# Kernel tuning notes

Hardware: AMD Instinct MI355X
Metric: run time of the kernel (lower is better)

## Reference

```python
import jax, jax.numpy as jnp
import numpy as np

N = 50000
E = 300000
F_IN, H, OUT = 100, 256, 512
L = 3


def _lin(key, fan_in, fan_out):
    k1, k2 = jax.random.split(key)
    lim = 1.0 / np.sqrt(fan_in)
    W = jax.random.uniform(k1, (fan_in, fan_out), minval=-lim, maxval=lim, dtype=jnp.float32)
    b = jax.random.uniform(k2, (fan_out,), minval=-lim, maxval=lim, dtype=jnp.float32)
    return W, b


def setup_inputs() -> dict:
    key = jax.random.key(0)
    ks = jax.random.split(key, 12)
    x = jax.random.normal(ks[0], (N, F_IN), dtype=jnp.float32)
    edge_index = jax.random.randint(ks[1], (2, E), 0, N, dtype=jnp.int64)
    edge_attr = jax.random.uniform(ks[2], (E,), dtype=jnp.float32)
    Wi, bi = _lin(ks[3], F_IN, H)
    gW, gb = [], []
    for i in range(L):
        W, b = _lin(ks[4 + i], H, H)
        gW.append(W); gb.append(b)
    Wg = jnp.stack(gW)  # [L, H, H]
    bg = jnp.stack(gb)  # [L, H]
    Wo1, bo1 = _lin(ks[7], H, 2 * H)
    Wo2, bo2 = _lin(ks[8], 2 * H, OUT)
    Wh1, bh1 = _lin(ks[9], OUT, 256)
    Wh2, bh2 = _lin(ks[10], 256, 128)
    Wh3, bh3 = _lin(ks[11], 128, 5)
    return {"x": x, "edge_index": edge_index, "edge_attr": edge_attr,
            "target_species_idx": 0,
            "Wi": Wi, "bi": bi, "Wg": Wg, "bg": bg,
            "Wo1": Wo1, "bo1": bo1, "Wo2": Wo2, "bo2": bo2,
            "Wh1": Wh1, "bh1": bh1, "Wh2": Wh2, "bh2": bh2, "Wh3": Wh3, "bh3": bh3}


def _gcn_conv(x, W, b, row, col, norm):
    # PyG GCNConv: x' = D^-1/2 (A+I) D^-1/2 (x W) + b (norm precomputed)
    h = x @ W                                   # [N, H]
    msg = norm[:, None] * h[row]                # gather sources  [E+N, H]
    out = jnp.zeros_like(h).at[col].add(msg)    # scatter to targets
    return out + b


def reference(x, edge_index, edge_attr, target_species_idx,
              Wi, bi, Wg, bg, Wo1, bo1, Wo2, bo2,
              Wh1, bh1, Wh2, bh2, Wh3, bh3):
    n = x.shape[0]
    loop = jnp.arange(n, dtype=edge_index.dtype)
    row = jnp.concatenate([edge_index[0], loop])   # sources (with self-loops)
    col = jnp.concatenate([edge_index[1], loop])   # targets
    ew = jnp.concatenate([edge_attr, jnp.ones((n,), dtype=x.dtype)])
    deg = jnp.zeros((n,), dtype=x.dtype).at[col].add(ew)
    dinv = jnp.where(deg > 0, jax.lax.rsqrt(deg), 0.0)
    norm = dinv[row] * ew * dinv[col]              # [E+N]

    h = jax.nn.relu(x @ Wi + bi)
    for i in range(L):
        h = _gcn_conv(h, Wg[i], bg[i], row, col, norm)
        if i < L - 1:
            h = jax.nn.relu(h)  # dropout is identity in eval mode
    h = jax.nn.relu(h @ Wo1 + bo1) @ Wo2 + bo2     # output_proj [N, OUT]
    t = h[target_species_idx]                      # [OUT]
    t = jax.nn.relu(t @ Wh1 + bh1)
    t = jax.nn.relu(t @ Wh2 + bh2)
    return t @ Wh3 + bh3                           # [5]
```

## Files before the change

kernel.cpp:

```cpp
#include <hip/hip_runtime.h>

#define HDIM 256
#define CAPN 4096
#define MAXDEG 64
#define NT 256


__device__ __forceinline__ float4 fma4(float s, float4 w, float4 a) {
  a.x = fmaf(s, w.x, a.x); a.y = fmaf(s, w.y, a.y);
  a.z = fmaf(s, w.z, a.z); a.w = fmaf(s, w.w, a.w);
  return a;
}

__device__ __forceinline__ int detect_stride(const int* __restrict__ ei, int E,
                                             int* s_st, int tid) {
  if (tid < 64) {
    bool nz = (tid < E) && (ei[2 * tid + 1] != 0);
    unsigned long long b = __ballot(nz);
    if (tid == 0) *s_st = (b != 0ULL) ? 1 : 2;
  }
  __syncthreads();
  return *s_st;
}

__device__ __forceinline__ void load_cols4(const int* __restrict__ ei, int E, int e0,
                                           int st, int c[4]) {
  if (st == 1) {
    int4 v = *(const int4*)&ei[E + e0];
    c[0] = v.x; c[1] = v.y; c[2] = v.z; c[3] = v.w;
  } else {
    int4 v1 = *(const int4*)&ei[(size_t)(E + e0) * 2];
    int4 v2 = *(const int4*)&ei[(size_t)(E + e0) * 2 + 4];
    c[0] = v1.x; c[1] = v1.z; c[2] = v2.x; c[3] = v2.z;
  }
}

__global__ void k_init(int* __restrict__ map, float* __restrict__ deg,
                       int* __restrict__ meta, int* __restrict__ nodeof,
                       int* __restrict__ dcnt, const int* __restrict__ tgt, int N) {
  int t = tgt[0];
  int gtid = blockIdx.x * blockDim.x + threadIdx.x, gsz = gridDim.x * blockDim.x;
  int4* m4 = (int4*)map;
  float4* d4 = (float4*)deg;
  int nv = N >> 2, tv = t >> 2, tl = t & 3;
  for (int i = gtid; i < nv; i += gsz) {
    int4 z = {0, 0, 0, 0};
    if (i == tv) (&z.x)[tl] = 7;
    m4[i] = z;
    d4[i] = make_float4(0.f, 0.f, 0.f, 0.f);
  }
  for (int i = (nv << 2) + gtid; i < N; i += gsz) { map[i] = (i == t) ? 7 : 0; deg[i] = 0.f; }
  int4* c4 = (int4*)dcnt;
  for (int i = gtid; i < 3 * CAPN / 4; i += gsz) c4[i] = make_int4(0, 0, 0, 0);
  if (gtid == 0) { meta[0] = 1; meta[10] = 0; nodeof[0] = t; }
}

__device__ __forceinline__ void expand_edge(const int* __restrict__ ei, int E, int st,
                                            int e, int mv, int l, int* __restrict__ meta,
                                            int* __restrict__ map, int* __restrict__ nodeof,
                                            int* __restrict__ dcnt, int* __restrict__ dstl) {
  if (mv >= 4 && (mv & 3) >= l) {
    int sv = (mv >> 2) - 1;
    int idx = atomicAdd(&dcnt[sv], 1);
    if (idx < MAXDEG) dstl[sv * MAXDEG + idx] = e;
    else atomicOr(&meta[10], 1);
    int r = ei[(size_t)e * st];
    if (atomicCAS(&map[r], 0, 1) == 0) {
      int ns = atomicAdd(&meta[0], 1);
      if (ns < CAPN) { nodeof[ns] = r; map[r] = ((ns + 1) << 2) | (l - 1); }
    }
  }
}

#define DEGB 128
__global__ void k_deg_exp3(const int* __restrict__ ei, const float* __restrict__ ea,
                           int E, int* __restrict__ meta, int* __restrict__ map,
                           int* __restrict__ nodeof, int* __restrict__ dcnt2,
                           int* __restrict__ dstl2, float* __restrict__ deg) {
  __shared__ int s_st;
  int tid = threadIdx.x;
  int st = detect_stride(ei, E, &s_st, tid);
  if (blockIdx.x < DEGB) {
    int stride = DEGB * NT * 4;
    for (int e0 = (blockIdx.x * NT + tid) * 4; e0 < E; e0 += stride) {
      int ne = E - e0;
      if (ne >= 4) {
        int c[4]; load_cols4(ei, E, e0, st, c);
        float4 w = *(const float4*)&ea[e0];
        atomicAdd(&deg[c[0]], w.x); atomicAdd(&deg[c[1]], w.y);
        atomicAdd(&deg[c[2]], w.z); atomicAdd(&deg[c[3]], w.w);
      } else {
        for (int k = 0; k < ne; ++k)
          atomicAdd(&deg[ei[(size_t)(E + e0 + k) * st]], ea[e0 + k]);
      }
    }
  } else {
    int stride = DEGB * NT * 4;
    for (int e0 = ((blockIdx.x - DEGB) * NT + tid) * 4; e0 < E; e0 += stride) {
      int ne = E - e0;
      if (ne >= 4) {
        int c[4]; load_cols4(ei, E, e0, st, c);
        for (int k = 0; k < 4; ++k)
          expand_edge(ei, E, st, e0 + k, map[c[k]], 3, meta, map, nodeof, dcnt2, dstl2);
      } else {
        for (int k = 0; k < ne; ++k) {
          int c = ei[(size_t)(E + e0 + k) * st];
          expand_edge(ei, E, st, e0 + k, map[c], 3, meta, map, nodeof, dcnt2, dstl2);
        }
      }
    }
  }
}

__global__ void k_exp4(const int* __restrict__ ei, int E, int* __restrict__ meta,
                       int* __restrict__ map, int* __restrict__ nodeof,
                       int* __restrict__ dcnt, int* __restrict__ dstl, int l) {
  __shared__ int s_st;
  int tid = threadIdx.x;
  int st = detect_stride(ei, E, &s_st, tid);
  int e0 = (blockIdx.x * NT + tid) * 4;
  if (e0 >= E) return;
  int ne = E - e0;
  if (ne >= 4) {
    int c[4]; load_cols4(ei, E, e0, st, c);
    for (int k = 0; k < 4; ++k)
      expand_edge(ei, E, st, e0 + k, map[c[k]], l, meta, map, nodeof, dcnt, dstl);
  } else {
    for (int k = 0; k < ne; ++k) {
      int c = ei[(size_t)(E + e0 + k) * st];
      expand_edge(ei, E, st, e0 + k, map[c], l, meta, map, nodeof, dcnt, dstl);
    }
  }
}

__global__ void __launch_bounds__(NT) k_l0q(
    const int* __restrict__ meta, const int* __restrict__ nodeof,
    const float* __restrict__ x, const float* __restrict__ Wi,
    const float* __restrict__ bi, const float* __restrict__ W0,
    float* __restrict__ gout) {
  __shared__ float xs[4][112];
  __shared__ float hs[4][HDIM];
  __shared__ float4 red[4][4][64];
  const float4* Wi4 = (const float4*)Wi;
  const float4* W04 = (const float4*)W0;
  const float4* bi4 = (const float4*)bi;
  float4* g4 = (float4*)gout;
  int ntot = meta[0]; if (ntot > CAPN) ntot = CAPN;
  int tid = threadIdx.x, q = tid & 63, kg = tid >> 6;
  for (int base = blockIdx.x * 4; base < ntot; base += gridDim.x * 4) {
    int nr = ntot - base; if (nr > 4) nr = 4;
    for (int idx = tid; idx < nr * 100; idx += NT) {
      int r = idx / 100, k2 = idx - r * 100;
      xs[r][k2] = x[(size_t)nodeof[base + r] * 100 + k2];
    }
    __syncthreads();
    {
      float4 a0 = {0,0,0,0}, a1 = a0, a2 = a0, a3 = a0;
#pragma unroll 5
      for (int k2 = kg * 25; k2 < kg * 25 + 25; ++k2) {
        float4 w = Wi4[(size_t)k2 * 64 + q];
        a0 = fma4(xs[0][k2], w, a0); a1 = fma4(xs[1][k2], w, a1);
        a2 = fma4(xs[2][k2], w, a2); a3 = fma4(xs[3][k2], w, a3);
      }
      red[0][kg][q] = a0; red[1][kg][q] = a1; red[2][kg][q] = a2; red[3][kg][q] = a3;
    }
    __syncthreads();
    if (tid < 64) {
      float4 bb = bi4[tid];
      for (int r = 0; r < nr; ++r) {
        float4 s = red[r][0][tid], s1 = red[r][1][tid], s2 = red[r][2][tid], s3 = red[r][3][tid];
        s.x = fmaxf(s.x + s1.x + s2.x + s3.x + bb.x, 0.0f);
        s.y = fmaxf(s.y + s1.y + s2.y + s3.y + bb.y, 0.0f);
        s.z = fmaxf(s.z + s1.z + s2.z + s3.z + bb.z, 0.0f);
        s.w = fmaxf(s.w + s1.w + s2.w + s3.w + bb.w, 0.0f);
        *(float4*)&hs[r][tid * 4] = s;
      }
    }
    __syncthreads();
    {
      float4 a0 = {0,0,0,0}, a1 = a0, a2 = a0, a3 = a0;
#pragma unroll 4
      for (int m = kg * 64; m < kg * 64 + 64; ++m) {
        float4 w = W04[(size_t)m * 64 + q];
        a0 = fma4(hs[0][m], w, a0); a1 = fma4(hs[1][m], w, a1);
        a2 = fma4(hs[2][m], w, a2); a3 = fma4(hs[3][m], w, a3);
      }
      red[0][kg][q] = a0; red[1][kg][q] = a1; red[2][kg][q] = a2; red[3][kg][q] = a3;
    }
    __syncthreads();
    if (tid < 64) {
      for (int r = 0; r < nr; ++r) {
        float4 s = red[r][0][tid], s1 = red[r][1][tid], s2 = red[r][2][tid], s3 = red[r][3][tid];
        s.x += s1.x + s2.x + s3.x; s.y += s1.y + s2.y + s3.y;
        s.z += s1.z + s2.z + s3.z; s.w += s1.w + s2.w + s3.w;
        g4[(size_t)(base + r) * 64 + tid] = s;
      }
    }
    __syncthreads();
  }
}

__global__ void __launch_bounds__(NT) k_gv(
    const int* __restrict__ meta, int kk, const int* __restrict__ map,
    const int* __restrict__ nodeof, const int* __restrict__ ei, int E,
    const float* __restrict__ ea, const float* __restrict__ deg,
    const int* __restrict__ dcnt, const int* __restrict__ dstl,
    const float* __restrict__ gprev, const float* __restrict__ W,
    const float* __restrict__ bprev, float* __restrict__ gout) {
  __shared__ int s_st;
  __shared__ float hs[4][HDIM];
  __shared__ float4 red[4][4][64];
  __shared__ int   sul[4][MAXDEG];
  __shared__ float nrml[4][MAXDEG];
  __shared__ float dvr[4];
  __shared__ int   ml[4];
  int tid = threadIdx.x;
  int st = detect_stride(ei, E, &s_st, tid);
  const float4* W4 = (const float4*)W;
  const float4* b4 = (const float4*)bprev;
  const float4* gp4 = (const float4*)gprev;
  float4* go4 = (float4*)gout;
  int ntot = meta[0]; if (ntot > CAPN) ntot = CAPN;
  int q = tid & 63, kg = tid >> 6;
  for (int base = blockIdx.x * 4; base < ntot; base += gridDim.x * 4) {
    int nr = ntot - base; if (nr > 4) nr = 4;
    int maxb = -1;
    for (int r = 0; r < nr; ++r) maxb = max(maxb, map[nodeof[base + r]] & 3);
    if (maxb < kk) continue;
    {
      int r = tid >> 6, i = tid & 63;
      if (r < nr) {
        int s = base + r;
        int m = dcnt[s]; if (m > MAXDEG) m = MAXDEG;
        if (i == 0) { ml[r] = m; dvr[r] = 1.0f / sqrtf(deg[nodeof[s]] + 1.0f); }
        if (i < m) {
          int e = dstl[s * MAXDEG + i];
          int u = ei[(size_t)e * st];
          int mu = map[u];
          sul[r][i] = (mu >= 4) ? (mu >> 2) - 1 : 0;
          nrml[r][i] = (mu >= 4) ? (1.0f / sqrtf(deg[u] + 1.0f)) * ea[e] : 0.0f;
        }
      }
    }
    __syncthreads();
    for (int idx = tid; idx < nr * 64; idx += NT) {
      int r = idx >> 6, qq = idx & 63;
      int s = base + r;
      float dv = dvr[r], d2 = dv * dv;
      float4 gs = gp4[(size_t)s * 64 + qq];
      float4 acc = b4[qq];
      acc.x = fmaf(d2, gs.x, acc.x); acc.y = fmaf(d2, gs.y, acc.y);
      acc.z = fmaf(d2, gs.z, acc.z); acc.w = fmaf(d2, gs.w, acc.w);
      float4 ms = {0,0,0,0};
      int m = ml[r];
      for (int i = 0; i < m; ++i)
        ms = fma4(nrml[r][i], gp4[(size_t)sul[r][i] * 64 + qq], ms);
      acc.x = fmaxf(fmaf(dv, ms.x, acc.x), 0.0f);
      acc.y = fmaxf(fmaf(dv, ms.y, acc.y), 0.0f);
      acc.z = fmaxf(fmaf(dv, ms.z, acc.z), 0.0f);
      acc.w = fmaxf(fmaf(dv, ms.w, acc.w), 0.0f);
      *(float4*)&hs[r][qq * 4] = acc;
    }
    __syncthreads();
    {
      float4 a0 = {0,0,0,0}, a1 = a0, a2 = a0, a3 = a0;
#pragma unroll 4
      for (int m = kg * 64; m < kg * 64 + 64; ++m) {
        float4 w = W4[(size_t)m * 64 + q];
        a0 = fma4(hs[0][m], w, a0); a1 = fma4(hs[1][m], w, a1);
        a2 = fma4(hs[2][m], w, a2); a3 = fma4(hs[3][m], w, a3);
      }
      red[0][kg][q] = a0; red[1][kg][q] = a1; red[2][kg][q] = a2; red[3][kg][q] = a3;
    }
    __syncthreads();
    if (tid < 64) {
      for (int r = 0; r < nr; ++r) {
        float4 s = red[r][0][tid], s1 = red[r][1][tid], s2 = red[r][2][tid], s3 = red[r][3][tid];
        s.x += s1.x + s2.x + s3.x; s.y += s1.y + s2.y + s3.y;
        s.z += s1.z + s2.z + s3.z; s.w += s1.w + s2.w + s3.w;
        go4[(size_t)(base + r) * 64 + tid] = s;
      }
    }
    __syncthreads();
  }
}

__global__ void __launch_bounds__(NT) k_heads1(
    const int* __restrict__ ei, int E, const float* __restrict__ ea,
    const int* __restrict__ map, const int* __restrict__ nodeof,
    const int* __restrict__ dcnt2, const int* __restrict__ dstl2,
    const float* __restrict__ deg, const float* __restrict__ b2,
    const float* __restrict__ g2, const float* __restrict__ Wo1,
    const float* __restrict__ bo1, float* __restrict__ v1) {
  __shared__ int s_st;
  __shared__ float h3[256];
  __shared__ float4 red[256];
  __shared__ int   sul[MAXDEG];
  __shared__ float nrml[MAXDEG];
  int tid = threadIdx.x;
  int st = detect_stride(ei, E, &s_st, tid);
  int t = nodeof[0];
  float dvt = 1.0f / sqrtf(deg[t] + 1.0f);
  int m = dcnt2[0]; if (m > MAXDEG) m = MAXDEG;
  if (tid < m) {
    int e = dstl2[tid];
    int u = ei[(size_t)e * st];
    int mu = map[u];
    sul[tid] = (mu >= 4) ? (mu >> 2) - 1 : 0;
    nrml[tid] = (mu >= 4) ? (1.0f / sqrtf(deg[u] + 1.0f)) * ea[e] : 0.0f;
  }
  __syncthreads();
  {
    float acc = b2[tid] + dvt * dvt * g2[tid];
    float ms = 0.0f;
    for (int i = 0; i < m; ++i)
      ms = fmaf(nrml[i], g2[(size_t)sul[i] * HDIM + tid], ms);
    h3[tid] = fmaf(dvt, ms, acc);
  }
  __syncthreads();
  int q = tid & 15, kg = tid >> 4;
  const float4* W4 = (const float4*)Wo1;
  int quad = blockIdx.x * 16 + q;
  float4 a = {0,0,0,0};
#pragma unroll
  for (int k = kg * 16; k < kg * 16 + 16; ++k)
    a = fma4(h3[k], W4[(size_t)k * 128 + quad], a);
  red[kg * 16 + q] = a;
  __syncthreads();
  if (tid < 16) {
    float4 s = red[tid];
    for (int g = 1; g < 16; ++g) {
      float4 r = red[g * 16 + tid];
      s.x += r.x; s.y += r.y; s.z += r.z; s.w += r.w;
    }
    float4 bb = ((const float4*)bo1)[blockIdx.x * 16 + tid];
    s.x = fmaxf(s.x + bb.x, 0.f); s.y = fmaxf(s.y + bb.y, 0.f);
    s.z = fmaxf(s.z + bb.z, 0.f); s.w = fmaxf(s.w + bb.w, 0.f);
    ((float4*)v1)[blockIdx.x * 16 + tid] = s;
  }
}

template <int KIN, int KOUT, int BLOCKS, bool RELU>
__global__ void __launch_bounds__(NT) k_headv(const float* __restrict__ vin,
                                              const float* __restrict__ W,
                                              const float* __restrict__ b,
                                              float* __restrict__ vout) {
  constexpr int QPB = KOUT / (4 * BLOCKS);
  constexpr int KG = 256 / QPB;
  constexpr int KQ = KIN / KG;
  __shared__ float vs[KIN];
  __shared__ float4 red[256];
  int tid = threadIdx.x;
  for (int k = tid; k < KIN; k += NT) vs[k] = vin[k];
  __syncthreads();
  int q = tid % QPB, kg = tid / QPB;
  const float4* W4 = (const float4*)W;
  int quad = blockIdx.x * QPB + q;
  float4 a = {0,0,0,0};
#pragma unroll 8
  for (int k = kg * KQ; k < kg * KQ + KQ; ++k)
    a = fma4(vs[k], W4[(size_t)k * (KOUT / 4) + quad], a);
  red[kg * QPB + q] = a;
  __syncthreads();
  if (tid < QPB) {
    float4 s = red[tid];
    for (int g = 1; g < KG; ++g) {
      float4 r = red[g * QPB + tid];
      s.x += r.x; s.y += r.y; s.z += r.z; s.w += r.w;
    }
    float4 bb = ((const float4*)b)[blockIdx.x * QPB + tid];
    s.x += bb.x; s.y += bb.y; s.z += bb.z; s.w += bb.w;
    if (RELU) {
      s.x = fmaxf(s.x, 0.f); s.y = fmaxf(s.y, 0.f);
      s.z = fmaxf(s.z, 0.f); s.w = fmaxf(s.w, 0.f);
    }
    ((float4*)vout)[blockIdx.x * QPB + tid] = s;
  }
}

__global__ void __launch_bounds__(NT) k_tailq(
    const float* __restrict__ vin, const float* __restrict__ Wh2,
    const float* __restrict__ bh2, const float* __restrict__ Wh3,
    const float* __restrict__ bh3, const int* __restrict__ meta,
    float* __restrict__ out) {
  __shared__ float vs[256];
  __shared__ float4 red[256];
  __shared__ float v4s[128];
  int tid = threadIdx.x;
  vs[tid] = vin[tid];
  __syncthreads();
  int q = tid & 31, kg = tid >> 5;
  const float4* W4 = (const float4*)Wh2;
  float4 a = {0,0,0,0};
#pragma unroll 8
  for (int k = kg * 32; k < kg * 32 + 32; ++k)
    a = fma4(vs[k], W4[(size_t)k * 32 + q], a);
  red[kg * 32 + q] = a;
  __syncthreads();
  if (tid < 32) {
    float4 s = red[tid];
    for (int g = 1; g < 8; ++g) {
      float4 r = red[g * 32 + tid];
      s.x += r.x; s.y += r.y; s.z += r.z; s.w += r.w;
    }
    float4 bb = ((const float4*)bh2)[tid];
    *(float4*)&v4s[tid * 4] = make_float4(fmaxf(s.x + bb.x, 0.f), fmaxf(s.y + bb.y, 0.f),
                                          fmaxf(s.z + bb.z, 0.f), fmaxf(s.w + bb.w, 0.f));
  }
  __syncthreads();
  if (tid < 5) {
    float a2 = bh3[tid];
#pragma unroll 4
    for (int k = 0; k < 128; ++k) a2 = fmaf(v4s[k], Wh3[k * 5 + tid], a2);
    if (tid == 4) {
      int B = 0;
      if (meta[0] > CAPN) B |= 1;
      if (meta[10] != 0) B |= 2;
      if (B) a2 = 1.0e6f * (float)B;
    }
    out[tid] = a2;
  }
}

__global__ void k_diag(float* __restrict__ out, float D) {
  int tid = threadIdx.x;
  if (tid < 4) out[tid] = 0.0f;
  if (tid == 4) out[tid] = D;
}

extern "C" void kernel_launch(void* const* d_in, const int* in_sizes, int n_in,
                              void* d_out, int out_size, void* d_ws, size_t ws_size,
                              hipStream_t stream) {
  float* out = (float*)d_out;

  static const long long EXP[18] = {5000000, 600000, 300000, 1, 25600, 256, 196608, 768,
                                    131072, 512, 262144, 512, 131072, 256, 32768, 128, 640, 5};
  if (n_in != 18) {
    k_diag<<<1, 64, 0, stream>>>(out, 3.0e6f + 1000.0f * (float)n_in);
    return;
  }
  for (int i = 0; i < 18; ++i) {
    long long s = in_sizes[i];
    bool ok = (s == EXP[i]) || (i == 1 && s == 2 * EXP[1]);
    if (!ok) {
      k_diag<<<1, 64, 0, stream>>>(out, (float)(i + 1) * 1.0e5f);
      return;
    }
  }

  const float* x   = (const float*)d_in[0];
  const int*   ei  = (const int*)d_in[1];
  const float* ea  = (const float*)d_in[2];
  const int*   tgt = (const int*)d_in[3];
  const float* Wi  = (const float*)d_in[4];
  const float* bi  = (const float*)d_in[5];
  const float* Wg  = (const float*)d_in[6];
  const float* bg  = (const float*)d_in[7];
  const float* Wo1 = (const float*)d_in[8];
  const float* bo1 = (const float*)d_in[9];
  const float* Wo2 = (const float*)d_in[10];
  const float* bo2 = (const float*)d_in[11];
  const float* Wh1 = (const float*)d_in[12];
  const float* bh1 = (const float*)d_in[13];
  const float* Wh2 = (const float*)d_in[14];
  const float* bh2 = (const float*)d_in[15];
  const float* Wh3 = (const float*)d_in[16];
  const float* bh3 = (const float*)d_in[17];

  const int N = 50000, E = 300000;

  auto al = [](size_t b) { return (b + 255) & ~(size_t)255; };
  char* ws = (char*)d_ws;
  size_t off = 0;
  auto alloc = [&](size_t bytes) { char* p = ws + off; off += al(bytes); return p; };

  int*   map    = (int*)alloc((size_t)N * 4);
  int*   meta   = (int*)alloc(256);
  float* deg    = (float*)alloc((size_t)N * 4);
  int*   nodeof = (int*)alloc((size_t)CAPN * 4);
  int*   dcnt   = (int*)alloc((size_t)3 * CAPN * 4);
  int*   dstl   = (int*)alloc((size_t)3 * CAPN * MAXDEG * 4);
  float* gA     = (float*)alloc((size_t)CAPN * HDIM * 4);
  float* gB     = (float*)alloc((size_t)CAPN * HDIM * 4);
  float* headv  = (float*)alloc(8192);
  float* v1 = headv;
  float* v2 = headv + 512;
  float* v3 = headv + 1024;

  if (off > ws_size) {
    k_diag<<<1, 64, 0, stream>>>(out, 9.0e6f + (float)(ws_size >> 20));
    return;
  }

  int* dcnt0 = dcnt;               int* dstl0 = dstl;
  int* dcnt1 = dcnt + CAPN;        int* dstl1 = dstl + (size_t)CAPN * MAXDEG;
  int* dcnt2 = dcnt + 2 * CAPN;    int* dstl2 = dstl + (size_t)2 * CAPN * MAXDEG;

  dim3 b256(NT);
  int gE4 = (E + NT * 4 - 1) / (NT * 4);

  k_init<<<128, b256, 0, stream>>>(map, deg, meta, nodeof, dcnt, tgt, N);
  k_deg_exp3<<<256, b256, 0, stream>>>(ei, ea, E, meta, map, nodeof, dcnt2, dstl2, deg);
  k_exp4<<<gE4, b256, 0, stream>>>(ei, E, meta, map, nodeof, dcnt1, dstl1, 2);
  k_exp4<<<gE4, b256, 0, stream>>>(ei, E, meta, map, nodeof, dcnt0, dstl0, 1);

  k_l0q<<<128, b256, 0, stream>>>(meta, nodeof, x, Wi, bi, Wg, gA);
  k_gv<<<64, b256, 0, stream>>>(meta, 1, map, nodeof, ei, E, ea, deg, dcnt0, dstl0,
                                gA, Wg + (size_t)1 * HDIM * HDIM, bg, gB);
  k_gv<<<64, b256, 0, stream>>>(meta, 2, map, nodeof, ei, E, ea, deg, dcnt1, dstl1,
                                gB, Wg + (size_t)2 * HDIM * HDIM, bg + HDIM, gA);

  k_heads1<<<8, b256, 0, stream>>>(ei, E, ea, map, nodeof, dcnt2, dstl2, deg,
                                   bg + 2 * HDIM, gA, Wo1, bo1, v1);
  k_headv<512, 512, 16, false><<<16, b256, 0, stream>>>(v1, Wo2, bo2, v2);
  k_headv<512, 256, 8, true ><<<8, b256, 0, stream>>>(v2, Wh1, bh1, v3);
  k_tailq<<<1, b256, 0, stream>>>(v3, Wh2, bh2, Wh3, bh3, meta, out);
}
```

Before: 82.25 us.

## Shrink receptive-field expansion to two hops and push-scatter layer-0 contributions

Instead of expanding the target's 3-hop neighbourhood and running the input projection plus layer 0 on every node in it, only two hops are expanded. The layer-0 aggregation into 1-hop nodes is computed by an edge-scanning kernel that projects each contributing source and atomically scatters normalised results. Layers 1 and 2 and the first output projection are fused into one kernel that keeps the small 2-hop set in shared memory. This removes one full edge pass and the large per-node dense work, at the cost of per-edge serial matvecs inside blocks and tight capacity limits flagged through sentinel outputs.

After: 106.3 us. +29.2%, slower.

```diff
diff --git a/kernel.cpp b/kernel.cpp
--- a/kernel.cpp
+++ b/kernel.cpp
@@ -1,8 +1,11 @@
 #include <hip/hip_runtime.h>
 
 #define HDIM 256
-#define CAPN 4096
-#define MAXDEG 64
+#define CAPS1 512
+#define CAPS2 16
+#define B1CAP 64
+#define B2CAP 64
+#define QCAP  64
 #define NT 256
 
 
@@ -36,52 +39,39 @@
 }
 
 __global__ void k_init(int* __restrict__ map, float* __restrict__ deg,
+                       float* __restrict__ h1, int* __restrict__ dcnt1,
                        int* __restrict__ meta, int* __restrict__ nodeof,
-                       int* __restrict__ dcnt, const int* __restrict__ tgt, int N) {
+                       const int* __restrict__ tgt, int N) {
   int t = tgt[0];
   int gtid = blockIdx.x * blockDim.x + threadIdx.x, gsz = gridDim.x * blockDim.x;
-  int4* m4 = (int4*)map;
-  float4* d4 = (float4*)deg;
+  int4* m4 = (int4*)map; float4* d4 = (float4*)deg; float4* h4 = (float4*)h1;
   int nv = N >> 2, tv = t >> 2, tl = t & 3;
+  float4 zf = {0.f, 0.f, 0.f, 0.f};
   for (int i = gtid; i < nv; i += gsz) {
     int4 z = {0, 0, 0, 0};
-    if (i == tv) (&z.x)[tl] = 7;
-    m4[i] = z;
-    d4[i] = make_float4(0.f, 0.f, 0.f, 0.f);
-  }
-  for (int i = (nv << 2) + gtid; i < N; i += gsz) { map[i] = (i == t) ? 7 : 0; deg[i] = 0.f; }
-  int4* c4 = (int4*)dcnt;
-  for (int i = gtid; i < 3 * CAPN / 4; i += gsz) c4[i] = make_int4(0, 0, 0, 0);
-  if (gtid == 0) { meta[0] = 1; meta[10] = 0; nodeof[0] = t; }
-}
-
-__device__ __forceinline__ void expand_edge(const int* __restrict__ ei, int E, int st,
-                                            int e, int mv, int l, int* __restrict__ meta,
-                                            int* __restrict__ map, int* __restrict__ nodeof,
-                                            int* __restrict__ dcnt, int* __restrict__ dstl) {
-  if (mv >= 4 && (mv & 3) >= l) {
-    int sv = (mv >> 2) - 1;
-    int idx = atomicAdd(&dcnt[sv], 1);
-    if (idx < MAXDEG) dstl[sv * MAXDEG + idx] = e;
-    else atomicOr(&meta[10], 1);
-    int r = ei[(size_t)e * st];
-    if (atomicCAS(&map[r], 0, 1) == 0) {
-      int ns = atomicAdd(&meta[0], 1);
-      if (ns < CAPN) { nodeof[ns] = r; map[r] = ((ns + 1) << 2) | (l - 1); }
-    }
+    if (i == tv) (&z.x)[tl] = 1;
+    m4[i] = z; d4[i] = zf;
+  }
+  for (int i = (nv << 2) + gtid; i < N; i += gsz) { map[i] = (i == t) ? 1 : 0; deg[i] = 0.f; }
+  for (int i = gtid; i < CAPS1 * HDIM / 4; i += gsz) h4[i] = zf;
+  if (gtid < 32) dcnt1[gtid] = 0;
+  if (gtid == 0) {
+    for (int i = 0; i < 16; ++i) meta[i] = 0;
+    meta[2] = 1;
+    nodeof[0] = t;
   }
 }
 
 #define DEGB 128
 __global__ void k_deg_exp3(const int* __restrict__ ei, const float* __restrict__ ea,
                            int E, int* __restrict__ meta, int* __restrict__ map,
-                           int* __restrict__ nodeof, int* __restrict__ dcnt2,
-                           int* __restrict__ dstl2, float* __restrict__ deg) {
+                           int* __restrict__ nodeof, int* __restrict__ dstl2,
+                           float* __restrict__ deg) {
   __shared__ int s_st;
   int tid = threadIdx.x;
   int st = detect_stride(ei, E, &s_st, tid);
+  int stride = DEGB * NT * 4;
   if (blockIdx.x < DEGB) {
-    int stride = DEGB * NT * 4;
     for (int e0 = (blockIdx.x * NT + tid) * 4; e0 < E; e0 += stride) {
       int ne = E - e0;
       if (ne >= 4) {
@@ -95,248 +85,297 @@
       }
     }
   } else {
-    int stride = DEGB * NT * 4;
     for (int e0 = ((blockIdx.x - DEGB) * NT + tid) * 4; e0 < E; e0 += stride) {
-      int ne = E - e0;
-      if (ne >= 4) {
-        int c[4]; load_cols4(ei, E, e0, st, c);
-        for (int k = 0; k < 4; ++k)
-          expand_edge(ei, E, st, e0 + k, map[c[k]], 3, meta, map, nodeof, dcnt2, dstl2);
-      } else {
-        for (int k = 0; k < ne; ++k) {
-          int c = ei[(size_t)(E + e0 + k) * st];
-          expand_edge(ei, E, st, e0 + k, map[c], 3, meta, map, nodeof, dcnt2, dstl2);
+      int ne = E - e0; if (ne > 4) ne = 4;
+      int c[4];
+      if (ne == 4) load_cols4(ei, E, e0, st, c);
+      else for (int k = 0; k < ne; ++k) c[k] = ei[(size_t)(E + e0 + k) * st];
+      for (int k = 0; k < ne; ++k) {
+        if (map[c[k]] == 1) {
+          int e = e0 + k;
+          int idx = atomicAdd(&meta[3], 1);
+          if (idx < B2CAP) dstl2[idx] = e; else atomicOr(&meta[10], 1);
+          int r = ei[(size_t)e * st];
+          if (atomicCAS(&map[r], 0, -1) == 0) {
+            int ns = atomicAdd(&meta[2], 1);
+            if (ns < CAPS2) { nodeof[ns] = r; map[r] = ns + 1; }
+            else { if (ns < CAPS1) nodeof[ns] = r; atomicOr(&meta[10], 2); }
+          }
         }
       }
     }
   }
 }
 
-__global__ void k_exp4(const int* __restrict__ ei, int E, int* __restrict__ meta,
-                       int* __restrict__ map, int* __restrict__ nodeof,
-                       int* __restrict__ dcnt, int* __restrict__ dstl, int l) {
+__global__ void k_exp2(const int* __restrict__ ei, int E, const float* __restrict__ ea,
+                       int* __restrict__ meta, int* __restrict__ map,
+                       int* __restrict__ nodeof, int* __restrict__ dcnt1,
+                       int* __restrict__ dstl1) {
   __shared__ int s_st;
   int tid = threadIdx.x;
   int st = detect_stride(ei, E, &s_st, tid);
+  int n2 = meta[2]; if (n2 > CAPS2) n2 = CAPS2;
+  int n2base = meta[2];
   int e0 = (blockIdx.x * NT + tid) * 4;
   if (e0 >= E) return;
-  int ne = E - e0;
-  if (ne >= 4) {
-    int c[4]; load_cols4(ei, E, e0, st, c);
-    for (int k = 0; k < 4; ++k)
-      expand_edge(ei, E, st, e0 + k, map[c[k]], l, meta, map, nodeof, dcnt, dstl);
-  } else {
-    for (int k = 0; k < ne; ++k) {
-      int c = ei[(size_t)(E + e0 + k) * st];
-      expand_edge(ei, E, st, e0 + k, map[c], l, meta, map, nodeof, dcnt, dstl);
-    }
-  }
-}
-
-__global__ void __launch_bounds__(NT) k_l0q(
-    const int* __restrict__ meta, const int* __restrict__ nodeof,
+  int ne = E - e0; if (ne > 4) ne = 4;
+  int c[4];
+  if (ne == 4) load_cols4(ei, E, e0, st, c);
+  else for (int k = 0; k < ne; ++k) c[k] = ei[(size_t)(E + e0 + k) * st];
+  for (int k = 0; k < ne; ++k) {
+    int mv = map[c[k]];
+    if (mv > 0 && mv <= n2) {
+      int e = e0 + k, sv = mv - 1;
+      int idx = atomicAdd(&dcnt1[sv], 1);
+      if (idx < B1CAP) dstl1[sv * B1CAP + idx] = e; else atomicOr(&meta[10], 1);
+      int r = ei[(size_t)e * st];
+      if (atomicCAS(&map[r], 0, -1) == 0) {
+        int slot = n2base + atomicAdd(&meta[1], 1);
+        if (slot < CAPS1) { nodeof[slot] = r; map[r] = slot + 1; }
+        else atomicOr(&meta[10], 2);
+      }
+    }
+  }
+}
+
+#define SCANB 448
+__global__ void __launch_bounds__(NT) k_scan1l0(
+    const int* __restrict__ ei, int E, const float* __restrict__ ea,
+    int* __restrict__ meta, const int* __restrict__ map,
+    const int* __restrict__ nodeof, const float* __restrict__ deg,
     const float* __restrict__ x, const float* __restrict__ Wi,
     const float* __restrict__ bi, const float* __restrict__ W0,
-    float* __restrict__ gout) {
-  __shared__ float xs[4][112];
-  __shared__ float hs[4][HDIM];
-  __shared__ float4 red[4][4][64];
+    float* __restrict__ h1) {
+  __shared__ int s_st, qn;
+  __shared__ int qu[QCAP], qs[QCAP];
+  __shared__ float qnrm[QCAP];
+  __shared__ float xs[112];
+  __shared__ float hs[HDIM];
+  __shared__ float4 red[4][64];
+  int tid = threadIdx.x;
+  int st = detect_stride(ei, E, &s_st, tid);
+  if (tid == 0) qn = 0;
+  __syncthreads();
+  int n1 = meta[2] + meta[1]; if (n1 > CAPS1) n1 = CAPS1;
+  if (blockIdx.x < SCANB) {
+    int chunk = (E + SCANB - 1) / SCANB;
+    int lo = blockIdx.x * chunk, hi = lo + chunk; if (hi > E) hi = E;
+    for (int e = lo + tid; e < hi; e += NT) {
+      int c = ei[(size_t)(E + e) * st];
+      int mv = map[c];
+      if (mv > 0 && mv - 1 < n1) {
+        int u = ei[(size_t)e * st];
+        float nrm = rsqrtf(deg[u] + 1.0f) * ea[e] * rsqrtf(deg[c] + 1.0f);
+        int p = atomicAdd(&qn, 1);
+        if (p < QCAP) { qu[p] = u; qs[p] = mv - 1; qnrm[p] = nrm; }
+        else atomicOr(&meta[10], 4);
+      }
+    }
+  } else if (tid == 0) {
+    for (int s = blockIdx.x - SCANB; s < n1; s += 64) {
+      int u = nodeof[s];
+      float dv = rsqrtf(deg[u] + 1.0f);
+      int p = atomicAdd(&qn, 1);
+      if (p < QCAP) { qu[p] = u; qs[p] = s; qnrm[p] = dv * dv; }
+      else atomicOr(&meta[10], 4);
+    }
+  }
+  __syncthreads();
+  int qm = qn; if (qm > QCAP) qm = QCAP;
   const float4* Wi4 = (const float4*)Wi;
   const float4* W04 = (const float4*)W0;
   const float4* bi4 = (const float4*)bi;
-  float4* g4 = (float4*)gout;
-  int ntot = meta[0]; if (ntot > CAPN) ntot = CAPN;
-  int tid = threadIdx.x, q = tid & 63, kg = tid >> 6;
-  for (int base = blockIdx.x * 4; base < ntot; base += gridDim.x * 4) {
-    int nr = ntot - base; if (nr > 4) nr = 4;
-    for (int idx = tid; idx < nr * 100; idx += NT) {
-      int r = idx / 100, k2 = idx - r * 100;
-      xs[r][k2] = x[(size_t)nodeof[base + r] * 100 + k2];
+  int q = tid & 63, kg = tid >> 6;
+  for (int i = 0; i < qm; ++i) {
+    int u = qu[i], sv = qs[i];
+    float nrm = qnrm[i];
+    if (tid < 100) xs[tid] = x[(size_t)u * 100 + tid];
+    __syncthreads();
+    float4 a = {0, 0, 0, 0};
+#pragma unroll 5
+    for (int k2 = kg * 25; k2 < kg * 25 + 25; ++k2)
+      a = fma4(xs[k2], Wi4[(size_t)k2 * 64 + q], a);
+    red[kg][q] = a;
+    __syncthreads();
+    if (tid < 64) {
+      float4 s0 = red[0][tid], s1 = red[1][tid], s2 = red[2][tid], s3 = red[3][tid];
+      float4 bb = bi4[tid];
+      float4 h;
+      h.x = fmaxf(s0.x + s1.x + s2.x + s3.x + bb.x, 0.0f);
+      h.y = fmaxf(s0.y + s1.y + s2.y + s3.y + bb.y, 0.0f);
+      h.z = fmaxf(s0.z + s1.z + s2.z + s3.z + bb.z, 0.0f);
+      h.w = fmaxf(s0.w + s1.w + s2.w + s3.w + bb.w, 0.0f);
+      *(float4*)&hs[tid * 4] = h;
+    }
+    __syncthreads();
+    a = make_float4(0, 0, 0, 0);
+#pragma unroll 4
+    for (int m = kg * 64; m < kg * 64 + 64; ++m)
+      a = fma4(hs[m], W04[(size_t)m * 64 + q], a);
+    red[kg][q] = a;
+    __syncthreads();
+    if (tid < 64) {
+      float4 s0 = red[0][tid], s1 = red[1][tid], s2 = red[2][tid], s3 = red[3][tid];
+      s0.x += s1.x + s2.x + s3.x; s0.y += s1.y + s2.y + s3.y;
+      s0.z += s1.z + s2.z + s3.z; s0.w += s1.w + s2.w + s3.w;
+      float* dst = &h1[(size_t)sv * HDIM + tid * 4];
+      atomicAdd(dst + 0, nrm * s0.x); atomicAdd(dst + 1, nrm * s0.y);
+      atomicAdd(dst + 2, nrm * s0.z); atomicAdd(dst + 3, nrm * s0.w);
+    }
+    __syncthreads();
+  }
+}
+
+__global__ void __launch_bounds__(NT) k_gv1(
+    const int* __restrict__ meta, const float* __restrict__ h1,
+    const float* __restrict__ b0, const float* __restrict__ W1,
+    float* __restrict__ g1) {
+  __shared__ float hs[4][HDIM];
+  __shared__ float4 red[4][4][16];
+  const float4* W4 = (const float4*)W1;
+  const float4* b4 = (const float4*)b0;
+  const float4* h4 = (const float4*)h1;
+  float4* g4 = (float4*)g1;
+  int n1 = meta[2] + meta[1]; if (n1 > CAPS1) n1 = CAPS1;
+  int tid = threadIdx.x;
+  int cg = blockIdx.x & 3, rb = blockIdx.x >> 2;
+  int tiles = (n1 + 3) >> 2;
+  for (int tile = rb; tile < tiles; tile += 16) {
+    int base = tile * 4, nr = n1 - base; if (nr > 4) nr = 4;
+    for (int idx = tid; idx < nr * 64; idx += NT) {
+      int r = idx >> 6, qq = idx & 63;
+      float4 hv = h4[(size_t)(base + r) * 64 + qq];
+      float4 bb = b4[qq];
+      hv.x = fmaxf(hv.x + bb.x, 0.f); hv.y = fmaxf(hv.y + bb.y, 0.f);
+      hv.z = fmaxf(hv.z + bb.z, 0.f); hv.w = fmaxf(hv.w + bb.w, 0.f);
+      *(float4*)&hs[r][qq * 4] = hv;
     }
     __syncthreads();
     {
-      float4 a0 = {0,0,0,0}, a1 = a0, a2 = a0, a3 = a0;
-#pragma unroll 5
-      for (int k2 = kg * 25; k2 < kg * 25 + 25; ++k2) {
-        float4 w = Wi4[(size_t)k2 * 64 + q];
-        a0 = fma4(xs[0][k2], w, a0); a1 = fma4(xs[1][k2], w, a1);
-        a2 = fma4(xs[2][k2], w, a2); a3 = fma4(xs[3][k2], w, a3);
-      }
-      red[0][kg][q] = a0; red[1][kg][q] = a1; red[2][kg][q] = a2; red[3][kg][q] = a3;
+      int c4 = tid & 15, r = (tid >> 4) & 3, ks = tid >> 6;
+      float4 a = {0, 0, 0, 0};
+#pragma unroll 8
+      for (int m = ks * 64; m < ks * 64 + 64; ++m)
+        a = fma4(hs[r][m], W4[(size_t)m * 64 + cg * 16 + c4], a);
+      red[ks][r][c4] = a;
     }
     __syncthreads();
     if (tid < 64) {
-      float4 bb = bi4[tid];
-      for (int r = 0; r < nr; ++r) {
-        float4 s = red[r][0][tid], s1 = red[r][1][tid], s2 = red[r][2][tid], s3 = red[r][3][tid];
-        s.x = fmaxf(s.x + s1.x + s2.x + s3.x + bb.x, 0.0f);
-        s.y = fmaxf(s.y + s1.y + s2.y + s3.y + bb.y, 0.0f);
-        s.z = fmaxf(s.z + s1.z + s2.z + s3.z + bb.z, 0.0f);
-        s.w = fmaxf(s.w + s1.w + s2.w + s3.w + bb.w, 0.0f);
-        *(float4*)&hs[r][tid * 4] = s;
-      }
-    }
-    __syncthreads();
-    {
-      float4 a0 = {0,0,0,0}, a1 = a0, a2 = a0, a3 = a0;
+      int rr = tid >> 4, cc = tid & 15;
+      float4 s = red[0][rr][cc], s1 = red[1][rr][cc], s2 = red[2][rr][cc], s3 = red[3][rr][cc];
+      s.x += s1.x + s2.x + s3.x; s.y += s1.y + s2.y + s3.y;
+      s.z += s1.z + s2.z + s3.z; s.w += s1.w + s2.w + s3.w;
+      if (rr < nr) g4[(size_t)(base + rr) * 64 + cg * 16 + cc] = s;
+    }
+    __syncthreads();
+  }
+}
+
+__global__ void __launch_bounds__(NT) k_gv2h1(
+    const int* __restrict__ ei, int E, const float* __restrict__ ea,
+    const int* __restrict__ meta, const int* __restrict__ map,
+    const int* __restrict__ nodeof, const float* __restrict__ deg,
+    const int* __restrict__ dcnt1, const int* __restrict__ dstl1,
+    const int* __restrict__ dstl2, const float* __restrict__ bg,
+    const float* __restrict__ g1, const float* __restrict__ W2,
+    const float* __restrict__ Wo1, const float* __restrict__ bo1,
+    float* __restrict__ v1) {
+  __shared__ int s_st;
+  __shared__ float h2s[CAPS2][HDIM];
+  __shared__ float g2s[CAPS2][HDIM];
+  __shared__ float4 red[4][4][64];
+  __shared__ float4 red1[256];
+  __shared__ float h3[HDIM];
+  __shared__ int sus[B1CAP];
+  __shared__ float nrms[B1CAP];
+  int tid = threadIdx.x;
+  int st = detect_stride(ei, E, &s_st, tid);
+  int n2 = meta[2]; if (n2 > CAPS2) n2 = CAPS2;
+  int n1 = meta[2] + meta[1]; if (n1 > CAPS1) n1 = CAPS1;
+  const float* b1 = bg + HDIM;
+  const float* b2 = bg + 2 * HDIM;
+  for (int s = 0; s < n2; ++s) {
+    int m = dcnt1[s]; if (m > B1CAP) m = B1CAP;
+    float dvs = rsqrtf(deg[nodeof[s]] + 1.0f);
+    if (tid < m) {
+      int e = dstl1[s * B1CAP + tid];
+      int u = ei[(size_t)e * st];
+      int mu = map[u];
+      bool ok = (mu > 0 && mu - 1 < n1);
+      sus[tid] = ok ? mu - 1 : 0;
+      nrms[tid] = ok ? rsqrtf(deg[u] + 1.0f) * ea[e] * dvs : 0.0f;
+    }
+    __syncthreads();
+    float acc = b1[tid] + dvs * dvs * g1[(size_t)s * HDIM + tid];
+    for (int i = 0; i < m; ++i)
+      acc = fmaf(nrms[i], g1[(size_t)sus[i] * HDIM + tid], acc);
+    h2s[s][tid] = fmaxf(acc, 0.0f);
+    __syncthreads();
+  }
+  const float4* W24 = (const float4*)W2;
+  int q = tid & 63, kg = tid >> 6;
+  for (int base = 0; base < n2; base += 4) {
+    int nr = n2 - base; if (nr > 4) nr = 4;
+    float4 a0 = {0,0,0,0}, a1 = a0, a2 = a0, a3 = a0;
 #pragma unroll 4
-      for (int m = kg * 64; m < kg * 64 + 64; ++m) {
-        float4 w = W04[(size_t)m * 64 + q];
-        a0 = fma4(hs[0][m], w, a0); a1 = fma4(hs[1][m], w, a1);
-        a2 = fma4(hs[2][m], w, a2); a3 = fma4(hs[3][m], w, a3);
-      }
-      red[0][kg][q] = a0; red[1][kg][q] = a1; red[2][kg][q] = a2; red[3][kg][q] = a3;
-    }
+    for (int m = kg * 64; m < kg * 64 + 64; ++m) {
+      float4 w = W24[(size_t)m * 64 + q];
+      a0 = fma4(h2s[base + 0][m], w, a0);
+      if (nr > 1) a1 = fma4(h2s[base + 1][m], w, a1);
+      if (nr > 2) a2 = fma4(h2s[base + 2][m], w, a2);
+      if (nr > 3) a3 = fma4(h2s[base + 3][m], w, a3);
+    }
+    red[0][kg][q] = a0; red[1][kg][q] = a1; red[2][kg][q] = a2; red[3][kg][q] = a3;
     __syncthreads();
     if (tid < 64) {
       for (int r = 0; r < nr; ++r) {
-        float4 s = red[r][0][tid], s1 = red[r][1][tid], s2 = red[r][2][tid], s3 = red[r][3][tid];
-        s.x += s1.x + s2.x + s3.x; s.y += s1.y + s2.y + s3.y;
-        s.z += s1.z + s2.z + s3.z; s.w += s1.w + s2.w + s3.w;
-        g4[(size_t)(base + r) * 64 + tid] = s;
+        float4 s0 = red[r][0][tid], s1 = red[r][1][tid], s2 = red[r][2][tid], s3 = red[r][3][tid];
+        s0.x += s1.x + s2.x + s3.x; s0.y += s1.y + s2.y + s3.y;
+        s0.z += s1.z + s2.z + s3.z; s0.w += s1.w + s2.w + s3.w;
+        *(float4*)&g2s[base + r][tid * 4] = s0;
       }
     }
     __syncthreads();
   }
-}
-
-__global__ void __launch_bounds__(NT) k_gv(
-    const int* __restrict__ meta, int kk, const int* __restrict__ map,
-    const int* __restrict__ nodeof, const int* __restrict__ ei, int E,
-    const float* __restrict__ ea, const float* __restrict__ deg,
-    const int* __restrict__ dcnt, const int* __restrict__ dstl,
-    const float* __restrict__ gprev, const float* __restrict__ W,
-    const float* __restrict__ bprev, float* __restrict__ gout) {
-  __shared__ int s_st;
-  __shared__ float hs[4][HDIM];
-  __shared__ float4 red[4][4][64];
-  __shared__ int   sul[4][MAXDEG];
-  __shared__ float nrml[4][MAXDEG];
-  __shared__ float dvr[4];
-  __shared__ int   ml[4];
-  int tid = threadIdx.x;
-  int st = detect_stride(ei, E, &s_st, tid);
-  const float4* W4 = (const float4*)W;
-  const float4* b4 = (const float4*)bprev;
-  const float4* gp4 = (const float4*)gprev;
-  float4* go4 = (float4*)gout;
-  int ntot = meta[0]; if (ntot > CAPN) ntot = CAPN;
-  int q = tid & 63, kg = tid >> 6;
-  for (int base = blockIdx.x * 4; base < ntot; base += gridDim.x * 4) {
-    int nr = ntot - base; if (nr > 4) nr = 4;
-    int maxb = -1;
-    for (int r = 0; r < nr; ++r) maxb = max(maxb, map[nodeof[base + r]] & 3);
-    if (maxb < kk) continue;
-    {
-      int r = tid >> 6, i = tid & 63;
-      if (r < nr) {
-        int s = base + r;
-        int m = dcnt[s]; if (m > MAXDEG) m = MAXDEG;
-        if (i == 0) { ml[r] = m; dvr[r] = 1.0f / sqrtf(deg[nodeof[s]] + 1.0f); }
-        if (i < m) {
-          int e = dstl[s * MAXDEG + i];
-          int u = ei[(size_t)e * st];
-          int mu = map[u];
-          sul[r][i] = (mu >= 4) ? (mu >> 2) - 1 : 0;
-          nrml[r][i] = (mu >= 4) ? (1.0f / sqrtf(deg[u] + 1.0f)) * ea[e] : 0.0f;
-        }
+  {
+    float dvt = rsqrtf(deg[nodeof[0]] + 1.0f);
+    int m2 = meta[3]; if (m2 > B2CAP) m2 = B2CAP;
+    if (tid < m2) {
+      int e = dstl2[tid];
+      int u = ei[(size_t)e * st];
+      int mu = map[u];
+      bool ok = (mu > 0 && mu - 1 < n2);
+      sus[tid] = ok ? mu - 1 : 0;
+      nrms[tid] = ok ? rsqrtf(deg[u] + 1.0f) * ea[e] : 0.0f;
+    }
+    __syncthreads();
+    float acc = b2[tid] + dvt * dvt * g2s[0][tid];
+    float ms = 0.0f;
+    for (int i = 0; i < m2; ++i) ms = fmaf(nrms[i], g2s[sus[i]][tid], ms);
+    h3[tid] = fmaf(dvt, ms, acc);
+  }
+  __syncthreads();
+  {
+    int q2 = tid & 15, kg2 = tid >> 4;
+    const float4* W4 = (const float4*)Wo1;
+    int quad = blockIdx.x * 16 + q2;
+    float4 a = {0, 0, 0, 0};
+#pragma unroll
+    for (int k = kg2 * 16; k < kg2 * 16 + 16; ++k)
+      a = fma4(h3[k], W4[(size_t)k * 128 + quad], a);
+    red1[kg2 * 16 + q2] = a;
+    __syncthreads();
+    if (tid < 16) {
+      float4 s = red1[tid];
+      for (int g = 1; g < 16; ++g) {
+        float4 r = red1[g * 16 + tid];
+        s.x += r.x; s.y += r.y; s.z += r.z; s.w += r.w;
       }
-    }
-    __syncthreads();
-    for (int idx = tid; idx < nr * 64; idx += NT) {
-      int r = idx >> 6, qq = idx & 63;
-      int s = base + r;
-      float dv = dvr[r], d2 = dv * dv;
-      float4 gs = gp4[(size_t)s * 64 + qq];
-      float4 acc = b4[qq];
-      acc.x = fmaf(d2, gs.x, acc.x); acc.y = fmaf(d2, gs.y, acc.y);
-      acc.z = fmaf(d2, gs.z, acc.z); acc.w = fmaf(d2, gs.w, acc.w);
-      float4 ms = {0,0,0,0};
-      int m = ml[r];
-      for (int i = 0; i < m; ++i)
-        ms = fma4(nrml[r][i], gp4[(size_t)sul[r][i] * 64 + qq], ms);
-      acc.x = fmaxf(fmaf(dv, ms.x, acc.x), 0.0f);
-      acc.y = fmaxf(fmaf(dv, ms.y, acc.y), 0.0f);
-      acc.z = fmaxf(fmaf(dv, ms.z, acc.z), 0.0f);
-      acc.w = fmaxf(fmaf(dv, ms.w, acc.w), 0.0f);
-      *(float4*)&hs[r][qq * 4] = acc;
-    }
-    __syncthreads();
-    {
-      float4 a0 = {0,0,0,0}, a1 = a0, a2 = a0, a3 = a0;
-#pragma unroll 4
-      for (int m = kg * 64; m < kg * 64 + 64; ++m) {
-        float4 w = W4[(size_t)m * 64 + q];
-        a0 = fma4(hs[0][m], w, a0); a1 = fma4(hs[1][m], w, a1);
-        a2 = fma4(hs[2][m], w, a2); a3 = fma4(hs[3][m], w, a3);
-      }
-      red[0][kg][q] = a0; red[1][kg][q] = a1; red[2][kg][q] = a2; red[3][kg][q] = a3;
-    }
-    __syncthreads();
-    if (tid < 64) {
-      for (int r = 0; r < nr; ++r) {
-        float4 s = red[r][0][tid], s1 = red[r][1][tid], s2 = red[r][2][tid], s3 = red[r][3][tid];
-        s.x += s1.x + s2.x + s3.x; s.y += s1.y + s2.y + s3.y;
-        s.z += s1.z + s2.z + s3.z; s.w += s1.w + s2.w + s3.w;
-        go4[(size_t)(base + r) * 64 + tid] = s;
-      }
-    }
-    __syncthreads();
-  }
-}
-
-__global__ void __launch_bounds__(NT) k_heads1(
-    const int* __restrict__ ei, int E, const float* __restrict__ ea,
-    const int* __restrict__ map, const int* __restrict__ nodeof,
-    const int* __restrict__ dcnt2, const int* __restrict__ dstl2,
-    const float* __restrict__ deg, const float* __restrict__ b2,
-    const float* __restrict__ g2, const float* __restrict__ Wo1,
-    const float* __restrict__ bo1, float* __restrict__ v1) {
-  __shared__ int s_st;
-  __shared__ float h3[256];
-  __shared__ float4 red[256];
-  __shared__ int   sul[MAXDEG];
-  __shared__ float nrml[MAXDEG];
-  int tid = threadIdx.x;
-  int st = detect_stride(ei, E, &s_st, tid);
-  int t = nodeof[0];
-  float dvt = 1.0f / sqrtf(deg[t] + 1.0f);
-  int m = dcnt2[0]; if (m > MAXDEG) m = MAXDEG;
-  if (tid < m) {
-    int e = dstl2[tid];
-    int u = ei[(size_t)e * st];
-    int mu = map[u];
-    sul[tid] = (mu >= 4) ? (mu >> 2) - 1 : 0;
-    nrml[tid] = (mu >= 4) ? (1.0f / sqrtf(deg[u] + 1.0f)) * ea[e] : 0.0f;
-  }
-  __syncthreads();
-  {
-    float acc = b2[tid] + dvt * dvt * g2[tid];
-    float ms = 0.0f;
-    for (int i = 0; i < m; ++i)
-      ms = fmaf(nrml[i], g2[(size_t)sul[i] * HDIM + tid], ms);
-    h3[tid] = fmaf(dvt, ms, acc);
-  }
-  __syncthreads();
-  int q = tid & 15, kg = tid >> 4;
-  const float4* W4 = (const float4*)Wo1;
-  int quad = blockIdx.x * 16 + q;
-  float4 a = {0,0,0,0};
-#pragma unroll
-  for (int k = kg * 16; k < kg * 16 + 16; ++k)
-    a = fma4(h3[k], W4[(size_t)k * 128 + quad], a);
-  red[kg * 16 + q] = a;
-  __syncthreads();
-  if (tid < 16) {
-    float4 s = red[tid];
-    for (int g = 1; g < 16; ++g) {
-      float4 r = red[g * 16 + tid];
-      s.x += r.x; s.y += r.y; s.z += r.z; s.w += r.w;
-    }
-    float4 bb = ((const float4*)bo1)[blockIdx.x * 16 + tid];
-    s.x = fmaxf(s.x + bb.x, 0.f); s.y = fmaxf(s.y + bb.y, 0.f);
-    s.z = fmaxf(s.z + bb.z, 0.f); s.w = fmaxf(s.w + bb.w, 0.f);
-    ((float4*)v1)[blockIdx.x * 16 + tid] = s;
+      float4 bb = ((const float4*)bo1)[blockIdx.x * 16 + tid];
+      s.x = fmaxf(s.x + bb.x, 0.f); s.y = fmaxf(s.y + bb.y, 0.f);
+      s.z = fmaxf(s.z + bb.z, 0.f); s.w = fmaxf(s.w + bb.w, 0.f);
+      ((float4*)v1)[blockIdx.x * 16 + tid] = s;
+    }
   }
 }
 
@@ -356,7 +395,7 @@
   int q = tid % QPB, kg = tid / QPB;
   const float4* W4 = (const float4*)W;
   int quad = blockIdx.x * QPB + q;
-  float4 a = {0,0,0,0};
+  float4 a = {0, 0, 0, 0};
 #pragma unroll 8
   for (int k = kg * KQ; k < kg * KQ + KQ; ++k)
     a = fma4(vs[k], W4[(size_t)k * (KOUT / 4) + quad], a);
@@ -391,7 +430,7 @@
   __syncthreads();
   int q = tid & 31, kg = tid >> 5;
   const float4* W4 = (const float4*)Wh2;
-  float4 a = {0,0,0,0};
+  float4 a = {0, 0, 0, 0};
 #pragma unroll 8
   for (int k = kg * 32; k < kg * 32 + 32; ++k)
     a = fma4(vs[k], W4[(size_t)k * 32 + q], a);
@@ -414,8 +453,8 @@
     for (int k = 0; k < 128; ++k) a2 = fmaf(v4s[k], Wh3[k * 5 + tid], a2);
     if (tid == 4) {
       int B = 0;
-      if (meta[0] > CAPN) B |= 1;
-      if (meta[10] != 0) B |= 2;
+      if (meta[2] > CAPS2 || meta[2] + meta[1] > CAPS1) B |= 1;
+      if (meta[3] > B2CAP || meta[10] != 0) B |= 2;
       if (B) a2 = 1.0e6f * (float)B;
     }
     out[tid] = a2;
@@ -475,13 +514,14 @@
   auto alloc = [&](size_t bytes) { char* p = ws + off; off += al(bytes); return p; };
 
   int*   map    = (int*)alloc((size_t)N * 4);
+  float* deg    = (float*)alloc((size_t)N * 4);
   int*   meta   = (int*)alloc(256);
-  float* deg    = (float*)alloc((size_t)N * 4);
-  int*   nodeof = (int*)alloc((size_t)CAPN * 4);
-  int*   dcnt   = (int*)alloc((size_t)3 * CAPN * 4);
-  int*   dstl   = (int*)alloc((size_t)3 * CAPN * MAXDEG * 4);
-  float* gA     = (float*)alloc((size_t)CAPN * HDIM * 4);
-  float* gB     = (float*)alloc((size_t)CAPN * HDIM * 4);
+  int*   nodeof = (int*)alloc((size_t)CAPS1 * 4);
+  int*   dstl2  = (int*)alloc((size_t)B2CAP * 4);
+  int*   dcnt1  = (int*)alloc(32 * 4);
+  int*   dstl1  = (int*)alloc((size_t)CAPS2 * B1CAP * 4);
+  float* h1     = (float*)alloc((size_t)CAPS1 * HDIM * 4);
+  float* g1     = (float*)alloc((size_t)CAPS1 * HDIM * 4);
   float* headv  = (float*)alloc(8192);
   float* v1 = headv;
   float* v2 = headv + 512;
@@ -492,26 +532,18 @@
     return;
   }
 
-  int* dcnt0 = dcnt;               int* dstl0 = dstl;
-  int* dcnt1 = dcnt + CAPN;        int* dstl1 = dstl + (size_t)CAPN * MAXDEG;
-  int* dcnt2 = dcnt + 2 * CAPN;    int* dstl2 = dstl + (size_t)2 * CAPN * MAXDEG;
-
   dim3 b256(NT);
   int gE4 = (E + NT * 4 - 1) / (NT * 4);
 
-  k_init<<<128, b256, 0, stream>>>(map, deg, meta, nodeof, dcnt, tgt, N);
-  k_deg_exp3<<<256, b256, 0, stream>>>(ei, ea, E, meta, map, nodeof, dcnt2, dstl2, deg);
-  k_exp4<<<gE4, b256, 0, stream>>>(ei, E, meta, map, nodeof, dcnt1, dstl1, 2);
-  k_exp4<<<gE4, b256, 0, stream>>>(ei, E, meta, map, nodeof, dcnt0, dstl0, 1);
-
-  k_l0q<<<128, b256, 0, stream>>>(meta, nodeof, x, Wi, bi, Wg, gA);
-  k_gv<<<64, b256, 0, stream>>>(meta, 1, map, nodeof, ei, E, ea, deg, dcnt0, dstl0,
-                                gA, Wg + (size_t)1 * HDIM * HDIM, bg, gB);
-  k_gv<<<64, b256, 0, stream>>>(meta, 2, map, nodeof, ei, E, ea, deg, dcnt1, dstl1,
-                                gB, Wg + (size_t)2 * HDIM * HDIM, bg + HDIM, gA);
-
-  k_heads1<<<8, b256, 0, stream>>>(ei, E, ea, map, nodeof, dcnt2, dstl2, deg,
-                                   bg + 2 * HDIM, gA, Wo1, bo1, v1);
+  k_init<<<128, b256, 0, stream>>>(map, deg, h1, dcnt1, meta, nodeof, tgt, N);
+  k_deg_exp3<<<256, b256, 0, stream>>>(ei, ea, E, meta, map, nodeof, dstl2, deg);
+  k_exp2<<<gE4, b256, 0, stream>>>(ei, E, ea, meta, map, nodeof, dcnt1, dstl1);
+  k_scan1l0<<<512, b256, 0, stream>>>(ei, E, ea, meta, map, nodeof, deg,
+                                      x, Wi, bi, Wg, h1);
+  k_gv1<<<64, b256, 0, stream>>>(meta, h1, bg, Wg + (size_t)1 * HDIM * HDIM, g1);
+  k_gv2h1<<<8, b256, 0, stream>>>(ei, E, ea, meta, map, nodeof, deg, dcnt1, dstl1,
+                                  dstl2, bg, g1, Wg + (size_t)2 * HDIM * HDIM,
+                                  Wo1, bo1, v1);
   k_headv<512, 512, 16, false><<<16, b256, 0, stream>>>(v1, Wo2, bo2, v2);
   k_headv<512, 256, 8, true ><<<8, b256, 0, stream>>>(v2, Wh1, bh1, v3);
   k_tailq<<<1, b256, 0, stream>>>(v3, Wh2, bh2, Wh3, bh3, meta, out);
```
